# Performance work log

Measured on AMD Instinct MI355X. Metric: run time of the kernel, lower is better.

Reference implementation:

```python
import jax, jax.numpy as jnp
import numpy as np

N = 100000
E = 1600000
D_IN = 128
D_H = 128
D_OUT = 40


def setup_inputs() -> dict:
    key = jax.random.key(0)
    ks = jax.random.split(key, 16)
    x = jax.random.normal(ks[0], (N, D_IN), dtype=jnp.float32)
    edge_src = jax.random.randint(ks[1], (E,), 0, N, dtype=jnp.int32)
    edge_dst = jax.random.randint(ks[2], (E,), 0, N, dtype=jnp.int32)

    def glorot(k, shape):
        fan_in, fan_out = shape[1], shape[0]
        lim = jnp.sqrt(6.0 / (fan_in + fan_out)).astype(jnp.float32)
        return jax.random.uniform(k, shape, jnp.float32, -lim, lim)

    # SAGEConv params: Wl acts on aggregated neighbors, Wr on root, plus bias.
    Wl0 = glorot(ks[3], (D_H, D_IN)); Wr0 = glorot(ks[4], (D_H, D_IN)); b0 = jnp.zeros((D_H,), jnp.float32)
    Wl1 = glorot(ks[5], (D_H, D_H));  Wr1 = glorot(ks[6], (D_H, D_H));  b1 = jnp.zeros((D_H,), jnp.float32)
    Wl2 = glorot(ks[7], (D_OUT, D_H)); Wr2 = glorot(ks[8], (D_OUT, D_H)); b2 = jnp.zeros((D_OUT,), jnp.float32)
    return {"x": x, "edge_src": edge_src, "edge_dst": edge_dst,
            "Wl0": Wl0, "Wr0": Wr0, "b0": b0,
            "Wl1": Wl1, "Wr1": Wr1, "b1": b1,
            "Wl2": Wl2, "Wr2": Wr2, "b2": b2}


def _mean_aggregate(x, edge_src, edge_dst, inv_deg):
    # adj_t @ x with mean reduce: sum neighbor feats into dst, divide by degree
    agg = jax.ops.segment_sum(x[edge_src], edge_dst, num_segments=N)
    return agg * inv_deg


def _sage_conv(x, edge_src, edge_dst, inv_deg, Wl, Wr, b):
    agg = _mean_aggregate(x, edge_src, edge_dst, inv_deg)
    return agg @ Wl.T + x @ Wr.T + b


def reference(x, edge_src, edge_dst, Wl0, Wr0, b0, Wl1, Wr1, b1, Wl2, Wr2, b2):
    deg = jax.ops.segment_sum(jnp.ones((E,), jnp.float32), edge_dst, num_segments=N)
    inv_deg = (1.0 / jnp.maximum(deg, 1.0))[:, None]  # [N,1]
    h = _sage_conv(x, edge_src, edge_dst, inv_deg, Wl0, Wr0, b0)
    h = jax.nn.relu(h)  # dropout is identity in eval mode
    h = _sage_conv(h, edge_src, edge_dst, inv_deg, Wl1, Wr1, b1)
    h = jax.nn.relu(h)
    h = _sage_conv(h, edge_src, edge_dst, inv_deg, Wl2, Wr2, b2)
    return jax.nn.log_softmax(h, axis=-1)
```

## Files before the change

### kernel.cpp

```cpp
#include <hip/hip_runtime.h>
#include <hip/hip_fp16.h>
#include <math.h>

#define NN 100000
#define NE 1600000
#define D 128
#define DOUT 40
#define NBUCK 391
#define CHUNK 4096
#define NCHUNK 391
#define EPT 16
#define LSTR 136

typedef _Float16 half8v __attribute__((ext_vector_type(8)));
typedef __attribute__((ext_vector_type(4))) float f32x4;

__device__ __forceinline__ unsigned packh(float a, float b) {
  return (unsigned)__half_as_ushort(__float2half_rn(a)) |
         ((unsigned)__half_as_ushort(__float2half_rn(b)) << 16);
}
__device__ __forceinline__ unsigned char f2fp8(float v) {
  return (unsigned char)(__builtin_amdgcn_cvt_pk_fp8_f32(v, v, 0, 0) & 0xff);
}
#define CVT2(u, s) __builtin_amdgcn_cvt_pk_f32_fp8((int)(u), s)
#define ACCR(v) { auto q = CVT2((v).x, 0); a[0] += q[0]; a[1] += q[1];   \
  q = CVT2((v).x, 1); a[2] += q[0];  a[3] += q[1];                        \
  q = CVT2((v).y, 0); a[4] += q[0];  a[5] += q[1];                        \
  q = CVT2((v).y, 1); a[6] += q[0];  a[7] += q[1];                        \
  q = CVT2((v).z, 0); a[8] += q[0];  a[9] += q[1];                        \
  q = CVT2((v).z, 1); a[10] += q[0]; a[11] += q[1];                       \
  q = CVT2((v).w, 0); a[12] += q[0]; a[13] += q[1];                       \
  q = CVT2((v).w, 1); a[14] += q[0]; a[15] += q[1]; }
#define ACCR8(v) { auto q = CVT2((v).x, 0); a[0] += q[0]; a[1] += q[1];  \
  q = CVT2((v).x, 1); a[2] += q[0]; a[3] += q[1];                         \
  q = CVT2((v).y, 0); a[4] += q[0]; a[5] += q[1];                         \
  q = CVT2((v).y, 1); a[6] += q[0]; a[7] += q[1]; }

__global__ void zero_kernel(int* __restrict__ p, int n) {
  int i = blockIdx.x * 256 + threadIdx.x;
  if (i < n) p[i] = 0;
}

__global__ __launch_bounds__(256) void cvt_kernel(const float* __restrict__ in,
                                                  _Float16* __restrict__ outh,
                                                  unsigned char* __restrict__ out8) {
  int i = (blockIdx.x * 256 + threadIdx.x) * 8;
  float4 v0 = *(const float4*)(in + i);
  float4 v1 = *(const float4*)(in + i + 4);
  uint4 oh;
  oh.x = packh(v0.x, v0.y);
  oh.y = packh(v0.z, v0.w);
  oh.z = packh(v1.x, v1.y);
  oh.w = packh(v1.z, v1.w);
  *(uint4*)(outh + i) = oh;
  unsigned w0 = __builtin_amdgcn_cvt_pk_fp8_f32(v0.x, v0.y, 0, 0);
  w0 = __builtin_amdgcn_cvt_pk_fp8_f32(v0.z, v0.w, w0, 1);
  unsigned w1 = __builtin_amdgcn_cvt_pk_fp8_f32(v1.x, v1.y, 0, 0);
  w1 = __builtin_amdgcn_cvt_pk_fp8_f32(v1.z, v1.w, w1, 1);
  *(uint2*)(out8 + i) = make_uint2(w0, w1);
}

__global__ __launch_bounds__(256) void bucket_hist_kernel(const int* __restrict__ dst,
                                                          int* __restrict__ bucket_cnt) {
  __shared__ int bc[NBUCK];
  int t = threadIdx.x;
  for (int i = t; i < NBUCK; i += 256) bc[i] = 0;
  __syncthreads();
  int e_base = blockIdx.x * CHUNK;
#pragma unroll
  for (int j = 0; j < EPT; ++j) {
    int e = e_base + j * 256 + t;
    if (e < NE) atomicAdd(&bc[dst[e] >> 8], 1);
  }
  __syncthreads();
  for (int i = t; i < NBUCK; i += 256)
    if (bc[i]) atomicAdd(&bucket_cnt[i], bc[i]);
}

__global__ __launch_bounds__(512) void bucket_scan_kernel(const int* __restrict__ bucket_cnt,
                                                          int* __restrict__ bucket_base,
                                                          int* __restrict__ bucket_cursor) {
  __shared__ int s[512];
  int t = threadIdx.x;
  int c = (t < NBUCK) ? bucket_cnt[t] : 0;
  s[t] = c;
  __syncthreads();
  for (int off = 1; off < 512; off <<= 1) {
    int v = (t >= off) ? s[t - off] : 0;
    __syncthreads();
    s[t] += v;
    __syncthreads();
  }
  if (t < NBUCK) {
    int b = s[t] - c;
    bucket_base[t] = b;
    bucket_cursor[t] = b;
  }
  if (t == NBUCK) bucket_base[NBUCK] = s[NBUCK - 1];
}

__global__ __launch_bounds__(256) void binned_scatter_kernel(const int* __restrict__ src,
                                                             const int* __restrict__ dst,
                                                             int* __restrict__ bucket_cursor,
                                                             unsigned* __restrict__ pairs) {
  __shared__ int lcnt[NBUCK];
  __shared__ int lscan[NBUCK];
  __shared__ int gb[NBUCK];
  __shared__ unsigned ebuf[CHUNK];
  __shared__ unsigned short bbuf[CHUNK];
  int t = threadIdx.x;
  int e_base = blockIdx.x * CHUNK;
  for (int i = t; i < NBUCK; i += 256) lcnt[i] = 0;
  __syncthreads();

  int myb[EPT], myrank[EPT];
  unsigned mye[EPT];
#pragma unroll
  for (int j = 0; j < EPT; ++j) {
    int e = e_base + j * 256 + t;
    if (e < NE) {
      int d = dst[e];
      mye[j] = (unsigned)src[e] | ((unsigned)(d & 255) << 24);
      myb[j] = d >> 8;
      myrank[j] = atomicAdd(&lcnt[d >> 8], 1);
    } else {
      myb[j] = -1;
    }
  }
  __syncthreads();

  lscan[t] = lcnt[t];
  if (256 + t < NBUCK) lscan[256 + t] = lcnt[256 + t];
  __syncthreads();
  for (int off = 1; off < 512; off <<= 1) {
    int v0 = (t >= off) ? lscan[t - off] : 0;
    int v1 = 0;
    int i1 = 256 + t;
    if (i1 < NBUCK) v1 = lscan[i1 - off];
    __syncthreads();
    if (t >= off) lscan[t] += v0;
    if (i1 < NBUCK) lscan[i1] += v1;
    __syncthreads();
  }

#pragma unroll
  for (int j = 0; j < EPT; ++j)
    if (myb[j] >= 0) {
      int b = myb[j];
      int lpos = lscan[b] - lcnt[b] + myrank[j];
      ebuf[lpos] = mye[j];
      bbuf[lpos] = (unsigned short)b;
    }
  for (int i = t; i < NBUCK; i += 256)
    if (lcnt[i] > 0) gb[i] = atomicAdd(&bucket_cursor[i], lcnt[i]);
  __syncthreads();

  int chunk_n = min(CHUNK, NE - e_base);
  for (int s2 = t; s2 < chunk_n; s2 += 256) {
    int b = bbuf[s2];
    int g = gb[b] + (s2 - (lscan[b] - lcnt[b]));
    pairs[g] = ebuf[s2];
  }
}

__global__ __launch_bounds__(256) void bucket_build_kernel(const unsigned* __restrict__ pairs,
                                                           const int* __restrict__ bucket_base,
                                                           int* __restrict__ row_start,
                                                           int* __restrict__ nbr,
                                                           float* __restrict__ inv_deg) {
  __shared__ int cnt[256], loc[256], cur[256];
  int b = blockIdx.x;
  int t = threadIdx.x;
  int nbase = b << 8;
  int e0 = bucket_base[b], e1 = bucket_base[b + 1];
  cnt[t] = 0;
  __syncthreads();
  for (int e = e0 + t; e < e1; e += 256) {
    int d = (int)(pairs[e] >> 24);
    atomicAdd(&cnt[d], 1);
  }
  __syncthreads();
  loc[t] = cnt[t];
  __syncthreads();
  for (int off = 1; off < 256; off <<= 1) {
    int v = (t >= off) ? loc[t - off] : 0;
    __syncthreads();
    loc[t] += v;
    __syncthreads();
  }
  int excl = loc[t] - cnt[t];
  int node = nbase + t;
  if (node < NN) {
    row_start[node] = e0 + excl;
    inv_deg[node] = 1.0f / (float)(cnt[t] > 1 ? cnt[t] : 1);
  }
  cur[t] = excl;
  if (b == NBUCK - 1 && t == 0) row_start[NN] = NE;
  __syncthreads();
  for (int e = e0 + t; e < e1; e += 256) {
    unsigned pr = pairs[e];
    int d = (int)(pr >> 24);
    int p = atomicAdd(&cur[d], 1);
    nbr[e0 + p] = (int)(pr & 0xFFFFFFu);
  }
}

__global__ __launch_bounds__(256) void agg_kernel(const unsigned char* __restrict__ X8,
                                                  _Float16* __restrict__ out,
                                                  const int* __restrict__ row_start,
                                                  const int* __restrict__ nbr,
                                                  const float* __restrict__ inv_deg) {
  int g = blockIdx.x * 32 + (threadIdx.x >> 3);
  int ln = threadIdx.x & 7;
  if (g >= NN) return;
  int p0 = row_start[g];
  int p1 = row_start[g + 1];
  const uint4* base = (const uint4*)X8;
  float a[16];
#pragma unroll
  for (int i = 0; i < 16; ++i) a[i] = 0.f;
  int p = p0;
  for (; p + 3 < p1; p += 4) {
    int s0 = nbr[p], s1 = nbr[p + 1], s2 = nbr[p + 2], s3 = nbr[p + 3];
    uint4 v0 = base[(size_t)s0 * 8 + ln];
    uint4 v1 = base[(size_t)s1 * 8 + ln];
    uint4 v2 = base[(size_t)s2 * 8 + ln];
    uint4 v3 = base[(size_t)s3 * 8 + ln];
    ACCR(v0) ACCR(v1) ACCR(v2) ACCR(v3)
  }
  for (; p < p1; ++p) {
    uint4 v = base[(size_t)nbr[p] * 8 + ln];
    ACCR(v)
  }
  float id = inv_deg[g];
  uint4 o0, o1;
  o0.x = packh(a[0] * id, a[1] * id);
  o0.y = packh(a[2] * id, a[3] * id);
  o0.z = packh(a[4] * id, a[5] * id);
  o0.w = packh(a[6] * id, a[7] * id);
  o1.x = packh(a[8] * id, a[9] * id);
  o1.y = packh(a[10] * id, a[11] * id);
  o1.z = packh(a[12] * id, a[13] * id);
  o1.w = packh(a[14] * id, a[15] * id);
  uint4* ob = (uint4*)out;
  ob[(size_t)g * 16 + ln * 2] = o0;
  ob[(size_t)g * 16 + ln * 2 + 1] = o1;
}

__global__ __launch_bounds__(64) void prep_w_kernel(const float* __restrict__ Wl,
                                                    const float* __restrict__ Wr,
                                                    half8v* __restrict__ P) {
  int s = blockIdx.x >> 3;
  int n = blockIdx.x & 7;
  int l = threadIdx.x;
  int k0 = s * 32 + (l >> 4) * 8;
  int c = n * 16 + (l & 15);
  const float* W = (k0 < 128) ? Wl : Wr;
  int kb = (k0 < 128) ? k0 : k0 - 128;
  half8v h;
#pragma unroll
  for (int i = 0; i < 8; ++i) h[i] = (_Float16)W[c * 128 + kb + i];
  P[blockIdx.x * 64 + l] = h;
}

__global__ __launch_bounds__(64) void prep_wy2_kernel(const float* __restrict__ Wl,
                                                      const float* __restrict__ Wr,
                                                      half8v* __restrict__ P) {
  int s = blockIdx.x / 5;
  int n = blockIdx.x % 5;
  int l = threadIdx.x;
  int k0 = s * 32 + (l >> 4) * 8;
  int c = n * 16 + (l & 15);
  const float* W = (c < DOUT) ? Wl : Wr;
  int row = (c < DOUT) ? c : c - DOUT;
  half8v h;
#pragma unroll
  for (int i = 0; i < 8; ++i) h[i] = (_Float16)W[row * 128 + k0 + i];
  P[blockIdx.x * 64 + l] = h;
}

__global__ __launch_bounds__(256) void mfma_gemm_kernel(
    const _Float16* __restrict__ A, const _Float16* __restrict__ H,
    const half8v* __restrict__ B, const float* __restrict__ bias,
    _Float16* __restrict__ out, unsigned char* __restrict__ out8) {
  __shared__ _Float16 Os[128][LSTR];

  int t = threadIdx.x;
  int w = t >> 6, l = t & 63;
  int R0 = blockIdx.x * 128;
  int lc = l & 15;
  int lg = l >> 4;

  int frow = R0 + w * 32 + lc;
  int fr0 = min(frow, NN - 1);
  int fr1 = min(frow + 16, NN - 1);

  f32x4 acc[2][8];
#pragma unroll
  for (int m = 0; m < 2; ++m)
#pragma unroll
    for (int n = 0; n < 8; ++n) acc[m][n] = (f32x4){0.f, 0.f, 0.f, 0.f};

#pragma unroll
  for (int s = 0; s < 8; ++s) {
    const _Float16* src = (s < 4) ? A : H;
    int koff = (s & 3) * 32 + lg * 8;
    half8v ah0 = *(const half8v*)(src + (size_t)fr0 * D + koff);
    half8v ah1 = *(const half8v*)(src + (size_t)fr1 * D + koff);
    half8v bh[8];
#pragma unroll
    for (int n = 0; n < 8; ++n) bh[n] = B[(s * 8 + n) * 64 + l];
#pragma unroll
    for (int n = 0; n < 8; ++n) {
      acc[0][n] = __builtin_amdgcn_mfma_f32_16x16x32_f16(ah0, bh[n], acc[0][n], 0, 0, 0);
      acc[1][n] = __builtin_amdgcn_mfma_f32_16x16x32_f16(ah1, bh[n], acc[1][n], 0, 0, 0);
    }
  }

  float bcol[8];
#pragma unroll
  for (int n = 0; n < 8; ++n) bcol[n] = bias[n * 16 + lc];
#pragma unroll
  for (int m = 0; m < 2; ++m)
#pragma unroll
    for (int n = 0; n < 8; ++n) {
      int col = n * 16 + lc;
#pragma unroll
      for (int j = 0; j < 4; ++j) {
        int row = w * 32 + m * 16 + lg * 4 + j;
        Os[row][col] = (_Float16)fmaxf(acc[m][n][j] + bcol[n], 0.f);
      }
    }
  __syncthreads();

#pragma unroll
  for (int i = 0; i < 8; ++i) {
    int u = t + 256 * i;
    int row = u >> 4, seg = u & 15;
    int gr = R0 + row;
    if (gr < NN) {
      uint4 v = *(const uint4*)&Os[row][seg * 8];
      *(uint4*)(out + (size_t)gr * D + seg * 8) = v;
      if (out8) {
        unsigned w0 = __builtin_amdgcn_cvt_pk_fp8_f32(
            __half2float(__ushort_as_half((unsigned short)(v.x & 0xffff))),
            __half2float(__ushort_as_half((unsigned short)(v.x >> 16))), 0, 0);
        w0 = __builtin_amdgcn_cvt_pk_fp8_f32(
            __half2float(__ushort_as_half((unsigned short)(v.y & 0xffff))),
            __half2float(__ushort_as_half((unsigned short)(v.y >> 16))), w0, 1);
        unsigned w1 = __builtin_amdgcn_cvt_pk_fp8_f32(
            __half2float(__ushort_as_half((unsigned short)(v.z & 0xffff))),
            __half2float(__ushort_as_half((unsigned short)(v.z >> 16))), 0, 0);
        w1 = __builtin_amdgcn_cvt_pk_fp8_f32(
            __half2float(__ushort_as_half((unsigned short)(v.w & 0xffff))),
            __half2float(__ushort_as_half((unsigned short)(v.w >> 16))), w1, 1);
        *(uint2*)(out8 + (size_t)gr * D + seg * 8) = make_uint2(w0, w1);
      }
    }
  }
}

__global__ __launch_bounds__(256) void mfma_y2_kernel(
    const _Float16* __restrict__ H, const half8v* __restrict__ B,
    const float* __restrict__ b2,
    unsigned char* __restrict__ yl8, float* __restrict__ yr) {
  __shared__ unsigned char Y8[128][64];
  __shared__ float Yr[128][40];

  int t = threadIdx.x;
  int w = t >> 6, l = t & 63;
  int R0 = blockIdx.x * 128;
  int lc = l & 15;
  int lg = l >> 4;

  int frow = R0 + w * 32 + lc;
  int fr0 = min(frow, NN - 1);
  int fr1 = min(frow + 16, NN - 1);

  f32x4 acc[2][5];
#pragma unroll
  for (int m = 0; m < 2; ++m)
#pragma unroll
    for (int n = 0; n < 5; ++n) acc[m][n] = (f32x4){0.f, 0.f, 0.f, 0.f};

#pragma unroll
  for (int s = 0; s < 4; ++s) {
    int koff = s * 32 + lg * 8;
    half8v ah0 = *(const half8v*)(H + (size_t)fr0 * D + koff);
    half8v ah1 = *(const half8v*)(H + (size_t)fr1 * D + koff);
    half8v bh[5];
#pragma unroll
    for (int n = 0; n < 5; ++n) bh[n] = B[(s * 5 + n) * 64 + l];
#pragma unroll
    for (int n = 0; n < 5; ++n) {
      acc[0][n] = __builtin_amdgcn_mfma_f32_16x16x32_f16(ah0, bh[n], acc[0][n], 0, 0, 0);
      acc[1][n] = __builtin_amdgcn_mfma_f32_16x16x32_f16(ah1, bh[n], acc[1][n], 0, 0, 0);
    }
  }

#pragma unroll
  for (int m = 0; m < 2; ++m)
#pragma unroll
    for (int n = 0; n < 5; ++n) {
      int col = n * 16 + lc;
#pragma unroll
      for (int j = 0; j < 4; ++j) {
        int row = w * 32 + m * 16 + lg * 4 + j;
        float v = acc[m][n][j];
        if (col < DOUT) {
          Y8[row][col] = f2fp8(v);
        } else {
          Yr[row][col - DOUT] = v + b2[col - DOUT];
        }
      }
    }
  if (t < 128) {
    *(uint2*)&Y8[t][40] = make_uint2(0, 0);
    *(uint2*)&Y8[t][48] = make_uint2(0, 0);
    *(uint2*)&Y8[t][56] = make_uint2(0, 0);
  }
  __syncthreads();

#pragma unroll
  for (int i = 0; i < 4; ++i) {
    int u = t + 256 * i;
    int row = u >> 3, seg = u & 7;
    int gr = R0 + row;
    if (gr < NN) *(uint2*)(yl8 + (size_t)gr * 64 + seg * 8) = *(const uint2*)&Y8[row][seg * 8];
  }
#pragma unroll
  for (int i = 0; i < 5; ++i) {
    int u = t + 256 * i;
    int row = u / 10, seg = u % 10;
    int gr = R0 + row;
    if (gr < NN) *(float4*)(yr + (size_t)gr * DOUT + seg * 4) = *(const float4*)&Yr[row][seg * 4];
  }
}

__global__ __launch_bounds__(256) void agg_out_kernel(const unsigned char* __restrict__ yl8,
                                                      const float* __restrict__ yr,
                                                      const int* __restrict__ row_start,
                                                      const int* __restrict__ nbr,
                                                      const float* __restrict__ inv_deg,
                                                      float* __restrict__ out) {
  int g = blockIdx.x * 32 + (threadIdx.x >> 3);
  int ln = threadIdx.x & 7;
  if (g >= NN) return;
  int p0 = row_start[g];
  int p1 = row_start[g + 1];
  const uint2* base = (const uint2*)yl8;
  float a[8];
#pragma unroll
  for (int i = 0; i < 8; ++i) a[i] = 0.f;
  int p = p0;
  for (; p + 3 < p1; p += 4) {
    int s0 = nbr[p], s1 = nbr[p + 1], s2 = nbr[p + 2], s3 = nbr[p + 3];
    uint2 v0 = base[(size_t)s0 * 8 + ln];
    uint2 v1 = base[(size_t)s1 * 8 + ln];
    uint2 v2 = base[(size_t)s2 * 8 + ln];
    uint2 v3 = base[(size_t)s3 * 8 + ln];
    ACCR8(v0) ACCR8(v1) ACCR8(v2) ACCR8(v3)
  }
  for (; p < p1; ++p) {
    uint2 v = base[(size_t)nbr[p] * 8 + ln];
    ACCR8(v)
  }
  float id = inv_deg[g];
  float z[8];
#pragma unroll
  for (int i = 0; i < 8; ++i) z[i] = a[i] * id;
  bool valid = (ln < 5);
  if (valid) {
    float4 r0 = *(const float4*)(yr + (size_t)g * DOUT + ln * 8);
    float4 r1 = *(const float4*)(yr + (size_t)g * DOUT + ln * 8 + 4);
    z[0] += r0.x; z[1] += r0.y; z[2] += r0.z; z[3] += r0.w;
    z[4] += r1.x; z[5] += r1.y; z[6] += r1.z; z[7] += r1.w;
  }
  float zm = -INFINITY;
  if (valid)
#pragma unroll
    for (int i = 0; i < 8; ++i) zm = fmaxf(zm, z[i]);
#pragma unroll
  for (int off = 1; off < 8; off <<= 1) zm = fmaxf(zm, __shfl_xor(zm, off, 8));
  float ssum = 0.f;
  if (valid)
#pragma unroll
    for (int i = 0; i < 8; ++i) ssum += expf(z[i] - zm);
#pragma unroll
  for (int off = 1; off < 8; off <<= 1) ssum += __shfl_xor(ssum, off, 8);
  float lse = zm + logf(ssum);
  if (valid) {
    float4 o0 = make_float4(z[0] - lse, z[1] - lse, z[2] - lse, z[3] - lse);
    float4 o1 = make_float4(z[4] - lse, z[5] - lse, z[6] - lse, z[7] - lse);
    *(float4*)(out + (size_t)g * DOUT + ln * 8) = o0;
    *(float4*)(out + (size_t)g * DOUT + ln * 8 + 4) = o1;
  }
}

extern "C" void kernel_launch(void* const* d_in, const int* in_sizes, int n_in,
                              void* d_out, int out_size, void* d_ws, size_t ws_size,
                              hipStream_t stream) {
  const float* x   = (const float*)d_in[0];
  const int* esrc  = (const int*)d_in[1];
  const int* edst  = (const int*)d_in[2];
  const float* Wl0 = (const float*)d_in[3];
  const float* Wr0 = (const float*)d_in[4];
  const float* b0  = (const float*)d_in[5];
  const float* Wl1 = (const float*)d_in[6];
  const float* Wr1 = (const float*)d_in[7];
  const float* b1  = (const float*)d_in[8];
  const float* Wl2 = (const float*)d_in[9];
  const float* Wr2 = (const float*)d_in[10];
  const float* b2  = (const float*)d_in[11];
  float* out = (float*)d_out;

  char* ws = (char*)d_ws;
  size_t off = 0;
  auto carve = [&](size_t bytes) -> char* {
    char* p = ws + off;
    off = (off + bytes + 255) & ~(size_t)255;
    return p;
  };
  int* bucket_cnt    = (int*)carve((size_t)NBUCK * 4);
  int* bucket_base   = (int*)carve((size_t)(NBUCK + 1) * 4);
  int* bucket_cursor = (int*)carve((size_t)NBUCK * 4);
  int* row_start     = (int*)carve((size_t)(NN + 1) * 4);
  int* nbr           = (int*)carve((size_t)NE * 4);
  float* inv_deg     = (float*)carve((size_t)NN * 4);
  unsigned* pairs    = (unsigned*)carve((size_t)NE * 4);
  half8v* B0         = (half8v*)carve((size_t)64 * 64 * 16);
  half8v* B1         = (half8v*)carve((size_t)64 * 64 * 16);
  half8v* By2        = (half8v*)carve((size_t)20 * 64 * 16);
  _Float16* xb   = (_Float16*)carve((size_t)NN * D * 2);
  unsigned char* x8    = (unsigned char*)carve((size_t)NN * D);
  _Float16* bufA = (_Float16*)carve((size_t)NN * D * 2);
  _Float16* bufB = (_Float16*)carve((size_t)NN * D * 2);
  unsigned char* bufB8 = (unsigned char*)carve((size_t)NN * D);
  _Float16* bufC = (_Float16*)carve((size_t)NN * D * 2);
  unsigned char* yl8   = (unsigned char*)carve((size_t)NN * 64);
  float* yr      = (float*)carve((size_t)NN * DOUT * 4);
  if (off > ws_size) return;

  const int GRID_AGG = (NN + 31) / 32;
  const int GRID_GEMM = (NN + 127) / 128;
  const int GRID_CVT = NN * D / 8 / 256;
  const int GRID_AO = (NN + 31) / 32;

  zero_kernel<<<2, 256, 0, stream>>>(bucket_cnt, NBUCK);
  bucket_hist_kernel<<<NCHUNK, 256, 0, stream>>>(edst, bucket_cnt);
  bucket_scan_kernel<<<1, 512, 0, stream>>>(bucket_cnt, bucket_base, bucket_cursor);
  binned_scatter_kernel<<<NCHUNK, 256, 0, stream>>>(esrc, edst, bucket_cursor, pairs);
  bucket_build_kernel<<<NBUCK, 256, 0, stream>>>(pairs, bucket_base, row_start, nbr, inv_deg);

  cvt_kernel<<<GRID_CVT, 256, 0, stream>>>(x, xb, x8);
  prep_w_kernel<<<64, 64, 0, stream>>>(Wl0, Wr0, B0);
  prep_w_kernel<<<64, 64, 0, stream>>>(Wl1, Wr1, B1);
  prep_wy2_kernel<<<20, 64, 0, stream>>>(Wl2, Wr2, By2);

  agg_kernel<<<GRID_AGG, 256, 0, stream>>>(x8, bufA, row_start, nbr, inv_deg);
  mfma_gemm_kernel<<<GRID_GEMM, 256, 0, stream>>>(bufA, xb, B0, b0, bufB, bufB8);
  agg_kernel<<<GRID_AGG, 256, 0, stream>>>(bufB8, bufA, row_start, nbr, inv_deg);
  mfma_gemm_kernel<<<GRID_GEMM, 256, 0, stream>>>(bufA, bufB, B1, b1, bufC, nullptr);
  mfma_y2_kernel<<<GRID_GEMM, 256, 0, stream>>>(bufC, By2, b2, yl8, yr);
  agg_out_kernel<<<GRID_AO, 256, 0, stream>>>(yl8, yr, row_start, nbr, inv_deg, out);
}
```

Before: 232.3 us.

## Fuse second SAGE GEMM with output projection GEMM through shared memory

Merges the layer-1 GEMM (with bias and ReLU) and the final 40-wide projection GEMM into one kernel. The ReLU'd fp16 hidden tile stays in LDS and feeds the second MFMA pass directly, so the full N×128 fp16 intermediate buffer is never written to or read back from global memory, and one kernel launch is removed. LDS is shared through a union between the hidden tile and the output staging, guarded by a barrier. In exchange the fused kernel uses more registers and LDS, which may lower occupancy.

```diff
diff --git a/kernel.cpp b/kernel.cpp
--- a/kernel.cpp
+++ b/kernel.cpp
@@ -341,31 +341,32 @@
     if (gr < NN) {
       uint4 v = *(const uint4*)&Os[row][seg * 8];
       *(uint4*)(out + (size_t)gr * D + seg * 8) = v;
-      if (out8) {
-        unsigned w0 = __builtin_amdgcn_cvt_pk_fp8_f32(
-            __half2float(__ushort_as_half((unsigned short)(v.x & 0xffff))),
-            __half2float(__ushort_as_half((unsigned short)(v.x >> 16))), 0, 0);
-        w0 = __builtin_amdgcn_cvt_pk_fp8_f32(
-            __half2float(__ushort_as_half((unsigned short)(v.y & 0xffff))),
-            __half2float(__ushort_as_half((unsigned short)(v.y >> 16))), w0, 1);
-        unsigned w1 = __builtin_amdgcn_cvt_pk_fp8_f32(
-            __half2float(__ushort_as_half((unsigned short)(v.z & 0xffff))),
-            __half2float(__ushort_as_half((unsigned short)(v.z >> 16))), 0, 0);
-        w1 = __builtin_amdgcn_cvt_pk_fp8_f32(
-            __half2float(__ushort_as_half((unsigned short)(v.w & 0xffff))),
-            __half2float(__ushort_as_half((unsigned short)(v.w >> 16))), w1, 1);
-        *(uint2*)(out8 + (size_t)gr * D + seg * 8) = make_uint2(w0, w1);
-      }
-    }
-  }
-}
-
-__global__ __launch_bounds__(256) void mfma_y2_kernel(
-    const _Float16* __restrict__ H, const half8v* __restrict__ B,
-    const float* __restrict__ b2,
+      unsigned w0 = __builtin_amdgcn_cvt_pk_fp8_f32(
+          __half2float(__ushort_as_half((unsigned short)(v.x & 0xffff))),
+          __half2float(__ushort_as_half((unsigned short)(v.x >> 16))), 0, 0);
+      w0 = __builtin_amdgcn_cvt_pk_fp8_f32(
+          __half2float(__ushort_as_half((unsigned short)(v.y & 0xffff))),
+          __half2float(__ushort_as_half((unsigned short)(v.y >> 16))), w0, 1);
+      unsigned w1 = __builtin_amdgcn_cvt_pk_fp8_f32(
+          __half2float(__ushort_as_half((unsigned short)(v.z & 0xffff))),
+          __half2float(__ushort_as_half((unsigned short)(v.z >> 16))), 0, 0);
+      w1 = __builtin_amdgcn_cvt_pk_fp8_f32(
+          __half2float(__ushort_as_half((unsigned short)(v.w & 0xffff))),
+          __half2float(__ushort_as_half((unsigned short)(v.w >> 16))), w1, 1);
+      *(uint2*)(out8 + (size_t)gr * D + seg * 8) = make_uint2(w0, w1);
+    }
+  }
+}
+
+__global__ __launch_bounds__(256) void mfma_gemm_out_kernel(
+    const _Float16* __restrict__ A, const _Float16* __restrict__ H,
+    const half8v* __restrict__ B, const float* __restrict__ bias,
+    const half8v* __restrict__ By2, const float* __restrict__ b2,
     unsigned char* __restrict__ yl8, float* __restrict__ yr) {
-  __shared__ unsigned char Y8[128][64];
-  __shared__ float Yr[128][40];
+  __shared__ union SM {
+    _Float16 Os[128][LSTR];
+    struct { unsigned char Y8[128][64]; float Yr[128][40]; } y;
+  } sm;
 
   int t = threadIdx.x;
   int w = t >> 6, l = t & 63;
@@ -377,26 +378,64 @@
   int fr0 = min(frow, NN - 1);
   int fr1 = min(frow + 16, NN - 1);
 
-  f32x4 acc[2][5];
+  f32x4 acc[2][8];
 #pragma unroll
   for (int m = 0; m < 2; ++m)
 #pragma unroll
-    for (int n = 0; n < 5; ++n) acc[m][n] = (f32x4){0.f, 0.f, 0.f, 0.f};
+    for (int n = 0; n < 8; ++n) acc[m][n] = (f32x4){0.f, 0.f, 0.f, 0.f};
+
+#pragma unroll
+  for (int s = 0; s < 8; ++s) {
+    const _Float16* src = (s < 4) ? A : H;
+    int koff = (s & 3) * 32 + lg * 8;
+    half8v ah0 = *(const half8v*)(src + (size_t)fr0 * D + koff);
+    half8v ah1 = *(const half8v*)(src + (size_t)fr1 * D + koff);
+    half8v bh[8];
+#pragma unroll
+    for (int n = 0; n < 8; ++n) bh[n] = B[(s * 8 + n) * 64 + l];
+#pragma unroll
+    for (int n = 0; n < 8; ++n) {
+      acc[0][n] = __builtin_amdgcn_mfma_f32_16x16x32_f16(ah0, bh[n], acc[0][n], 0, 0, 0);
+      acc[1][n] = __builtin_amdgcn_mfma_f32_16x16x32_f16(ah1, bh[n], acc[1][n], 0, 0, 0);
+    }
+  }
+
+  float bcol[8];
+#pragma unroll
+  for (int n = 0; n < 8; ++n) bcol[n] = bias[n * 16 + lc];
+#pragma unroll
+  for (int m = 0; m < 2; ++m)
+#pragma unroll
+    for (int n = 0; n < 8; ++n) {
+      int col = n * 16 + lc;
+#pragma unroll
+      for (int j = 0; j < 4; ++j) {
+        int row = w * 32 + m * 16 + lg * 4 + j;
+        sm.Os[row][col] = (_Float16)fmaxf(acc[m][n][j] + bcol[n], 0.f);
+      }
+    }
+
+  f32x4 acc2[2][5];
+#pragma unroll
+  for (int m = 0; m < 2; ++m)
+#pragma unroll
+    for (int n = 0; n < 5; ++n) acc2[m][n] = (f32x4){0.f, 0.f, 0.f, 0.f};
 
 #pragma unroll
   for (int s = 0; s < 4; ++s) {
     int koff = s * 32 + lg * 8;
-    half8v ah0 = *(const half8v*)(H + (size_t)fr0 * D + koff);
-    half8v ah1 = *(const half8v*)(H + (size_t)fr1 * D + koff);
+    half8v ah0 = *(const half8v*)&sm.Os[w * 32 + lc][koff];
+    half8v ah1 = *(const half8v*)&sm.Os[w * 32 + 16 + lc][koff];
     half8v bh[5];
 #pragma unroll
-    for (int n = 0; n < 5; ++n) bh[n] = B[(s * 5 + n) * 64 + l];
+    for (int n = 0; n < 5; ++n) bh[n] = By2[(s * 5 + n) * 64 + l];
 #pragma unroll
     for (int n = 0; n < 5; ++n) {
-      acc[0][n] = __builtin_amdgcn_mfma_f32_16x16x32_f16(ah0, bh[n], acc[0][n], 0, 0, 0);
-      acc[1][n] = __builtin_amdgcn_mfma_f32_16x16x32_f16(ah1, bh[n], acc[1][n], 0, 0, 0);
-    }
-  }
+      acc2[0][n] = __builtin_amdgcn_mfma_f32_16x16x32_f16(ah0, bh[n], acc2[0][n], 0, 0, 0);
+      acc2[1][n] = __builtin_amdgcn_mfma_f32_16x16x32_f16(ah1, bh[n], acc2[1][n], 0, 0, 0);
+    }
+  }
+  __syncthreads();
 
 #pragma unroll
   for (int m = 0; m < 2; ++m)
@@ -406,18 +445,18 @@
 #pragma unroll
       for (int j = 0; j < 4; ++j) {
         int row = w * 32 + m * 16 + lg * 4 + j;
-        float v = acc[m][n][j];
+        float v = acc2[m][n][j];
         if (col < DOUT) {
-          Y8[row][col] = f2fp8(v);
+          sm.y.Y8[row][col] = f2fp8(v);
         } else {
-          Yr[row][col - DOUT] = v + b2[col - DOUT];
+          sm.y.Yr[row][col - DOUT] = v + b2[col - DOUT];
         }
       }
     }
   if (t < 128) {
-    *(uint2*)&Y8[t][40] = make_uint2(0, 0);
-    *(uint2*)&Y8[t][48] = make_uint2(0, 0);
-    *(uint2*)&Y8[t][56] = make_uint2(0, 0);
+    *(uint2*)&sm.y.Y8[t][40] = make_uint2(0, 0);
+    *(uint2*)&sm.y.Y8[t][48] = make_uint2(0, 0);
+    *(uint2*)&sm.y.Y8[t][56] = make_uint2(0, 0);
   }
   __syncthreads();
 
@@ -426,14 +465,16 @@
     int u = t + 256 * i;
     int row = u >> 3, seg = u & 7;
     int gr = R0 + row;
-    if (gr < NN) *(uint2*)(yl8 + (size_t)gr * 64 + seg * 8) = *(const uint2*)&Y8[row][seg * 8];
+    if (gr < NN)
+      *(uint2*)(yl8 + (size_t)gr * 64 + seg * 8) = *(const uint2*)&sm.y.Y8[row][seg * 8];
   }
 #pragma unroll
   for (int i = 0; i < 5; ++i) {
     int u = t + 256 * i;
     int row = u / 10, seg = u % 10;
     int gr = R0 + row;
-    if (gr < NN) *(float4*)(yr + (size_t)gr * DOUT + seg * 4) = *(const float4*)&Yr[row][seg * 4];
+    if (gr < NN)
+      *(float4*)(yr + (size_t)gr * DOUT + seg * 4) = *(const float4*)&sm.y.Yr[row][seg * 4];
   }
 }
 
@@ -536,7 +577,6 @@
   _Float16* bufA = (_Float16*)carve((size_t)NN * D * 2);
   _Float16* bufB = (_Float16*)carve((size_t)NN * D * 2);
   unsigned char* bufB8 = (unsigned char*)carve((size_t)NN * D);
-  _Float16* bufC = (_Float16*)carve((size_t)NN * D * 2);
   unsigned char* yl8   = (unsigned char*)carve((size_t)NN * 64);
   float* yr      = (float*)carve((size_t)NN * DOUT * 4);
   if (off > ws_size) return;
@@ -560,7 +600,6 @@
   agg_kernel<<<GRID_AGG, 256, 0, stream>>>(x8, bufA, row_start, nbr, inv_deg);
   mfma_gemm_kernel<<<GRID_GEMM, 256, 0, stream>>>(bufA, xb, B0, b0, bufB, bufB8);
   agg_kernel<<<GRID_AGG, 256, 0, stream>>>(bufB8, bufA, row_start, nbr, inv_deg);
-  mfma_gemm_kernel<<<GRID_GEMM, 256, 0, stream>>>(bufA, bufB, B1, b1, bufC, nullptr);
-  mfma_y2_kernel<<<GRID_GEMM, 256, 0, stream>>>(bufC, By2, b2, yl8, yr);
+  mfma_gemm_out_kernel<<<GRID_GEMM, 256, 0, stream>>>(bufA, bufB, B1, b1, By2, b2, yl8, yr);
   agg_out_kernel<<<GRID_AO, 256, 0, stream>>>(yl8, yr, row_start, nbr, inv_deg, out);
 }
```

New measurement: 226.8 us. 2.4% less time.
